# Performance work log

Measured on AMD Instinct MI355X. Metric: run time of the kernel, lower is better.

The kernel has to match this reference:

```python
import jax, jax.numpy as jnp
import numpy as np

B, N, K = 8, 2048, 20
IN_CHAN = 3
CONV_DIMS = (64, 64, 128, 256)
FEAT_DIM = 1024
SLOPE = 0.2  # LeakyReLU negative slope (DGCNN standard)


def setup_inputs() -> dict:
    key = jax.random.key(0)
    ks = jax.random.split(key, 11)
    x = jax.random.normal(ks[0], (B, N, IN_CHAN), dtype=jnp.float32)
    in_dims = (IN_CHAN,) + CONV_DIMS[:-1]
    inp = {"x": x}
    for i, (cin, cout) in enumerate(zip(in_dims, CONV_DIMS)):
        inp[f"W{i+1}"] = jax.random.normal(ks[1 + 2 * i], (cout, 2 * cin), dtype=jnp.float32) * 0.05
        inp[f"b{i+1}"] = jnp.zeros((cout,), dtype=jnp.float32)
    inp["Wf"] = jax.random.normal(ks[9], (FEAT_DIM, sum(CONV_DIMS)), dtype=jnp.float32) * 0.05
    inp["bf"] = jnp.zeros((FEAT_DIM,), dtype=jnp.float32)
    return inp


def _knn_idx(x, k):
    # x: (B, N, C) -> indices of k nearest neighbors (self included), (B, N, K)
    xx = jnp.sum(x * x, axis=-1)                       # (B, N)
    inner = jnp.einsum('bnc,bmc->bnm', x, x)           # (B, N, N)
    d2 = xx[:, :, None] - 2.0 * inner + xx[:, None, :]  # squared distances
    _, idx = jax.lax.top_k(-d2, k)                     # k smallest distances
    return idx


def _edge_conv(x, W, b, k):
    # x: (B, N, C); W: (O, 2C); b: (O,) -> (B, N, O)
    idx = _knn_idx(x, k)                               # (B, N, K)
    nbr = jax.vmap(lambda xb, ib: xb[ib])(x, idx)      # (B, N, K, C) gather
    center = jnp.broadcast_to(x[:, :, None, :], nbr.shape)
    feat = jnp.concatenate([nbr - center, center], axis=-1)  # (B, N, K, 2C)
    h = jnp.einsum('bnkc,oc->bnko', feat, W) + b       # 1x1 conv over edges
    h = jax.nn.leaky_relu(h, SLOPE)
    return jnp.max(h, axis=2)                          # max over neighbors


def reference(x, W1, b1, W2, b2, W3, b3, W4, b4, Wf, bf):
    params = [(W1, b1), (W2, b2), (W3, b3), (W4, b4)]
    feats = []
    h = x
    for W, b in params:
        h = _edge_conv(h, W, b, K)
        feats.append(h)
    hcat = jnp.concatenate(feats, axis=-1)             # (B, N, sum(conv_dims))
    out = jnp.einsum('bnc,oc->bno', hcat, Wf) + bf     # final 1x1 conv
    out = jax.nn.leaky_relu(out, SLOPE)
    return jnp.max(out, axis=1)                        # global max pool -> (B, FEAT_DIM)
```

## Files before the change

kernel.cpp:

```cpp
#include <hip/hip_runtime.h>

constexpr int B_ = 8;
constexpr int N_ = 2048;
constexpr int K_ = 20;
constexpr float SLOPE_ = 0.2f;

typedef __attribute__((ext_vector_type(8))) short bf16x8;
typedef __attribute__((ext_vector_type(8))) _Float16 f16x8;
typedef __attribute__((ext_vector_type(4))) float f32x4;

__device__ __forceinline__ float lrelu(float v) { return v > 0.0f ? v : SLOPE_ * v; }

__device__ __forceinline__ void async16(const void* g, void* l) {
  __builtin_amdgcn_global_load_lds((const __attribute__((address_space(1))) unsigned int*)g,
                                   (__attribute__((address_space(3))) unsigned int*)l, 16, 0, 0);
}

__device__ __forceinline__ unsigned long long shflx64(unsigned long long v, int m) {
  return __shfl_xor(v, m, 64);
}

__device__ __forceinline__ unsigned short f2bf(float f) {
  unsigned u = __float_as_uint(f);
  u += 0x7fff + ((u >> 16) & 1);
  return (unsigned short)(u >> 16);
}

__device__ __forceinline__ unsigned short f2h(float f) {
  _Float16 h = (_Float16)f;
  return __builtin_bit_cast(unsigned short, h);
}
__device__ __forceinline__ float h2f(unsigned short u) {
  return (float)__builtin_bit_cast(_Float16, u);
}

__global__ void prep_wp(const float* __restrict__ W, float* __restrict__ Wp, int O, int C) {
  int i = blockIdx.x * 256 + threadIdx.x;
  if (i >= 2 * O * C) return;
  int o = i / C, c = i - o * C;
  if (o < O)
    Wp[i] = W[o * 2 * C + c];
  else
    Wp[i] = W[(o - O) * 2 * C + C + c] - W[(o - O) * 2 * C + c];
}

__global__ void cvt_bf16(const float4* __restrict__ src, ushort4* __restrict__ dst, int n4) {
  int i = blockIdx.x * 256 + threadIdx.x;
  if (i >= n4) return;
  float4 v = src[i];
  ushort4 o = {f2bf(v.x), f2bf(v.y), f2bf(v.z), f2bf(v.w)};
  dst[i] = o;
}

__global__ void norms_x(const float* __restrict__ x, float* __restrict__ xx) {
  int i = blockIdx.x * 256 + threadIdx.x;
  if (i >= B_ * N_) return;
  const float* p = x + (size_t)i * 3;
  xx[i] = p[0] * p[0] + p[1] * p[1] + p[2] * p[2];
}

__global__ void split32_x(const float* __restrict__ x, unsigned short* __restrict__ xh,
                          unsigned short* __restrict__ xm) {
  int id = blockIdx.x * 256 + threadIdx.x;
  if (id >= B_ * N_ * 32) return;
  int row = id >> 5, c = id & 31;
  float val = (c < 3) ? x[row * 3 + c] : 0.0f;
  unsigned short hb = f2h(val);
  float vh = h2f(hb);
  xh[id] = hb;
  xm[id] = f2h(val - vh);
}

template <int C>
__global__ void pack_knn(const unsigned short* __restrict__ Xh,
                         const unsigned short* __restrict__ Xm,
                         unsigned short* __restrict__ Pk) {
  constexpr int KK = C / 32;
  int id = blockIdx.x * 256 + threadIdx.x;
  const int outoff = id;
  const int l = id & 63;
  id >>= 6;
  const int split = id & 1;
  id >>= 1;
  const int kk = id % KK;
  id /= KK;
  const int tile = id & 127;
  const int b = id >> 7;
  const unsigned short* src = (split == 0) ? Xh : Xm;
  const size_t soff =
      (size_t)(b * N_ + tile * 16 + (l & 15)) * C + (size_t)kk * 32 + (size_t)(l >> 4) * 8;
  uint4 v = *(const uint4*)(src + soff);
  *(uint4*)(Pk + (size_t)outoff * 8) = v;
}

__device__ __forceinline__ void select_topk(const float* __restrict__ d2row, int lane,
                                            unsigned long long* __restrict__ cb,
                                            int* __restrict__ outp) {
  float r2[32];
#pragma unroll
  for (int i = 0; i < 32; i++) r2[i] = d2row[i * 64 + lane];

  const float INF = __int_as_float(0x7f800000);

  float lmin = r2[0];
#pragma unroll
  for (int i = 1; i < 32; i++) lmin = fminf(lmin, r2[i]);
  float sv = lmin;
#pragma unroll
  for (int k = 2; k <= 64; k <<= 1)
#pragma unroll
    for (int j = k >> 1; j > 0; j >>= 1) {
      float p = __shfl_xor(sv, j, 64);
      bool takeMax = ((lane & j) != 0) == ((lane & k) == 0);
      sv = takeMax ? fmaxf(sv, p) : fminf(sv, p);
    }
  float T = __shfl(sv, 19, 64);

  unsigned cnt = 0;
#pragma unroll
  for (int i = 0; i < 32; i++) {
    bool pred = r2[i] <= T;
    unsigned long long mk = __ballot(pred);
    if (mk) {
      int off = __popcll(mk & ((1ull << lane) - 1ull));
      unsigned pos = cnt + (unsigned)off;
      if (pred && pos < 64)
        cb[pos] = ((unsigned long long)__float_as_uint(r2[i]) << 32) | (unsigned)(i * 64 + lane);
      cnt += (unsigned)__popcll(mk);
    }
  }

  if (cnt <= 64) {
    unsigned long long v = (lane < (int)cnt) ? cb[lane] : ~0ull;
#pragma unroll
    for (int k = 2; k <= 64; k <<= 1)
#pragma unroll
      for (int j = k >> 1; j > 0; j >>= 1) {
        unsigned long long p = shflx64(v, j);
        bool takeMax = ((lane & j) != 0) == ((lane & k) == 0);
        bool lt = v < p;
        v = (takeMax == lt) ? p : v;
      }
    if (lane < K_) outp[lane] = (int)(unsigned)(v & 0xffffffffull);
  } else {
    for (int t2 = 0; t2 < K_; t2++) {
      unsigned long long loc = ~0ull;
#pragma unroll
      for (int i = 0; i < 32; i++) {
        unsigned long long u =
            ((unsigned long long)__float_as_uint(r2[i]) << 32) | (unsigned)(i * 64 + lane);
        loc = u < loc ? u : loc;
      }
#pragma unroll
      for (int off = 32; off > 0; off >>= 1) {
        unsigned long long vv = shflx64(loc, off);
        loc = vv < loc ? vv : loc;
      }
      const int mwin = (int)(unsigned)(loc & 0xffffffffull);
      if (lane == 0) outp[t2] = mwin;
#pragma unroll
      for (int i = 0; i < 32; i++)
        if (i * 64 + lane == mwin) r2[i] = INF;
    }
  }
}

template <int C>
__global__ __launch_bounds__(512, 2) void knn_mfma(const unsigned short* __restrict__ Pk,
                                                   const unsigned short* __restrict__ Xh,
                                                   const unsigned short* __restrict__ Xm,
                                                   const float* __restrict__ xx,
                                                   int* __restrict__ idxo) {
  constexpr int KK = C / 32;
  constexpr int NIT = KK * 16;
  const int b = blockIdx.x & 7;
  const int q0 = (blockIdx.x >> 3) * 32;
  const int tid = threadIdx.x;
  const int w = tid >> 6, lane = tid & 63;
  const int bN = b * N_;
  const int lr = lane & 15;
  const int lk = (lane >> 4) * 8;

  __shared__ float d2s[16][2052];
  __shared__ unsigned long long cbuf[8][64];

  const size_t qoff0 = (size_t)(bN + q0 + lr) * C + lk;
  const size_t qoff1 = (size_t)(bN + q0 + 16 + lr) * C + lk;

  f32x4 acc0[16], acc1[16];
#pragma unroll
  for (int t = 0; t < 16; t++) {
    acc0[t] = (f32x4){0.0f, 0.0f, 0.0f, 0.0f};
    acc1[t] = (f32x4){0.0f, 0.0f, 0.0f, 0.0f};
  }

  const size_t pbase = (size_t)b * (128 * KK * 2 * 512) + (size_t)lane * 8;
  f16x8 bh[2], bm[2];
#pragma unroll
  for (int i = 0; i < 2; i++) {
    const size_t a = pbase + (size_t)(((w * 16 + i) * KK + 0) * 2) * 512;
    bh[i] = *(const f16x8*)(Pk + a);
    bm[i] = *(const f16x8*)(Pk + a + 512);
  }
  f16x8 ah0, am0, ah1, am1;
#pragma unroll
  for (int it = 0; it < NIT; it++) {
    const int kk = it >> 4, t = it & 15, s = it & 1;
    if (t == 0) {
      ah0 = *(const f16x8*)(Xh + qoff0 + (size_t)kk * 32);
      am0 = *(const f16x8*)(Xm + qoff0 + (size_t)kk * 32);
      ah1 = *(const f16x8*)(Xh + qoff1 + (size_t)kk * 32);
      am1 = *(const f16x8*)(Xm + qoff1 + (size_t)kk * 32);
    }
    f16x8 vh = bh[s], vm = bm[s];
    if (it + 2 < NIT) {
      const int it2 = it + 2;
      const int kk2 = it2 >> 4, t2 = it2 & 15;
      const size_t a = pbase + (size_t)(((w * 16 + t2) * KK + kk2) * 2) * 512;
      bh[s] = *(const f16x8*)(Pk + a);
      bm[s] = *(const f16x8*)(Pk + a + 512);
    }
    acc0[t] = __builtin_amdgcn_mfma_f32_16x16x32_f16(ah0, vh, acc0[t], 0, 0, 0);
    acc0[t] = __builtin_amdgcn_mfma_f32_16x16x32_f16(ah0, vm, acc0[t], 0, 0, 0);
    acc0[t] = __builtin_amdgcn_mfma_f32_16x16x32_f16(am0, vh, acc0[t], 0, 0, 0);
    acc0[t] = __builtin_amdgcn_mfma_f32_16x16x32_f16(am0, vm, acc0[t], 0, 0, 0);
    acc1[t] = __builtin_amdgcn_mfma_f32_16x16x32_f16(ah1, vh, acc1[t], 0, 0, 0);
    acc1[t] = __builtin_amdgcn_mfma_f32_16x16x32_f16(ah1, vm, acc1[t], 0, 0, 0);
    acc1[t] = __builtin_amdgcn_mfma_f32_16x16x32_f16(am1, vh, acc1[t], 0, 0, 0);
    acc1[t] = __builtin_amdgcn_mfma_f32_16x16x32_f16(am1, vm, acc1[t], 0, 0, 0);
  }

  float qn0[4], qn1[4];
#pragma unroll
  for (int r = 0; r < 4; r++) {
    qn0[r] = xx[bN + q0 + (lane >> 4) * 4 + r];
    qn1[r] = xx[bN + q0 + 16 + (lane >> 4) * 4 + r];
  }

#pragma unroll
  for (int t = 0; t < 16; t++) {
    const int tt = w * 16 + t;
    float cn = xx[bN + tt * 16 + lr];
#pragma unroll
    for (int r = 0; r < 4; r++)
      d2s[(lane >> 4) * 4 + r][tt * 16 + lr] = fmaxf(fmaf(-2.0f, acc0[t][r], cn + qn0[r]), 0.0f);
  }
  __syncthreads();
  select_topk(&d2s[2 * w + 0][0], lane, cbuf[w], idxo + (size_t)(bN + q0 + 2 * w + 0) * K_);
  select_topk(&d2s[2 * w + 1][0], lane, cbuf[w], idxo + (size_t)(bN + q0 + 2 * w + 1) * K_);
  __syncthreads();

#pragma unroll
  for (int t = 0; t < 16; t++) {
    const int tt = w * 16 + t;
    float cn = xx[bN + tt * 16 + lr];
#pragma unroll
    for (int r = 0; r < 4; r++)
      d2s[(lane >> 4) * 4 + r][tt * 16 + lr] = fmaxf(fmaf(-2.0f, acc1[t][r], cn + qn1[r]), 0.0f);
  }
  __syncthreads();
  select_topk(&d2s[2 * w + 0][0], lane, cbuf[w], idxo + (size_t)(bN + q0 + 16 + 2 * w + 0) * K_);
  select_topk(&d2s[2 * w + 1][0], lane, cbuf[w], idxo + (size_t)(bN + q0 + 16 + 2 * w + 1) * K_);
}

template <int C, int O2>
__global__ void proj_kernel(const float* __restrict__ hin, int stride,
                            const float* __restrict__ Wp, float* __restrict__ P) {
  const int nt = (blockIdx.x & 7) * N_ + (blockIdx.x >> 3) * 16;
  const int o = blockIdx.y * blockDim.x + threadIdx.x;
  __shared__ float hs[16][C];
  for (int i = threadIdx.x; i < 16 * C; i += blockDim.x) {
    int r = i / C, c = i - r * C;
    hs[r][c] = hin[(size_t)(nt + r) * stride + c];
  }
  __syncthreads();
  float acc[16];
#pragma unroll
  for (int t = 0; t < 16; t++) acc[t] = 0.0f;
  const float* wr = Wp + (size_t)o * C;
  if constexpr (C % 4 == 0) {
    for (int cg = 0; cg < C; cg += 4) {
      float4 w = *(const float4*)(wr + cg);
#pragma unroll
      for (int t = 0; t < 16; t++) {
        float4 h = *(const float4*)(&hs[t][cg]);
        acc[t] += w.x * h.x + w.y * h.y + w.z * h.z + w.w * h.w;
      }
    }
  } else {
    for (int c = 0; c < C; c++) {
      float w = wr[c];
#pragma unroll
      for (int t = 0; t < 16; t++) acc[t] += w * hs[t][c];
    }
  }
#pragma unroll
  for (int t = 0; t < 16; t++) P[(size_t)(nt + t) * O2 + o] = acc[t];
}

__global__ __launch_bounds__(256) void gemm_proj(const unsigned short* __restrict__ A, int astride,
                                                 const unsigned short* __restrict__ Bw,
                                                 float* __restrict__ P) {
  const int m0 = ((blockIdx.x & 7) * 16 + (blockIdx.x >> 3)) * 128;
  const int n0 = blockIdx.y * 128;
  const int tid = threadIdx.x;
  const int w = tid >> 6, lane = tid & 63;
  const int wm = w & 1, wn = w >> 1;

  __shared__ unsigned short lA[128 * 32];
  __shared__ unsigned short lB[128 * 32];

  const int r0 = (w * 2 + 0) * 16 + (lane >> 2);
  const int r1 = (w * 2 + 1) * 16 + (lane >> 2);
  const int ks = (lane & 3) * 8;
  const unsigned short* a0 = A + (size_t)(m0 + r0) * astride + ks;
  const unsigned short* a1 = A + (size_t)(m0 + r1) * astride + ks;
  const unsigned short* b0 = Bw + (size_t)(n0 + r0) * 128 + ks;
  const unsigned short* b1 = Bw + (size_t)(n0 + r1) * 128 + ks;
  unsigned short* lA0 = lA + (w * 2 + 0) * 512;
  unsigned short* lA1 = lA + (w * 2 + 1) * 512;
  unsigned short* lB0 = lB + (w * 2 + 0) * 512;
  unsigned short* lB1 = lB + (w * 2 + 1) * 512;

  f32x4 acc[4][4] = {};
  const int ka = (lane >> 4) * 8;

  for (int k0 = 0; k0 < 128; k0 += 32) {
    __syncthreads();
    async16(a0 + k0, lA0);
    async16(a1 + k0, lA1);
    async16(b0 + k0, lB0);
    async16(b1 + k0, lB1);
    __syncthreads();
    bf16x8 af[4], bfr[4];
#pragma unroll
    for (int mt = 0; mt < 4; mt++)
      af[mt] = *(const bf16x8*)&lA[(wm * 64 + mt * 16 + (lane & 15)) * 32 + ka];
#pragma unroll
    for (int nt = 0; nt < 4; nt++)
      bfr[nt] = *(const bf16x8*)&lB[(wn * 64 + nt * 16 + (lane & 15)) * 32 + ka];
#pragma unroll
    for (int mt = 0; mt < 4; mt++)
#pragma unroll
      for (int nt = 0; nt < 4; nt++)
        acc[mt][nt] = __builtin_amdgcn_mfma_f32_16x16x32_bf16(af[mt], bfr[nt], acc[mt][nt], 0, 0, 0);
  }

  const int col = n0 + wn * 64 + (lane & 15);
  const int rowb = m0 + wm * 64 + (lane >> 4) * 4;
#pragma unroll
  for (int mt = 0; mt < 4; mt++)
#pragma unroll
    for (int nt = 0; nt < 4; nt++)
#pragma unroll
      for (int r = 0; r < 4; r++)
        P[(size_t)(rowb + mt * 16 + r) * 512 + col + nt * 16] = acc[mt][nt][r];
}

template <int O>
__global__ __launch_bounds__(256) void combine_kernel(
    const float* __restrict__ P, const int* __restrict__ idxo, const float* __restrict__ bias,
    float* __restrict__ hout, float* __restrict__ xxo, unsigned short* __restrict__ xh,
    unsigned short* __restrict__ xm, unsigned short* __restrict__ a4) {
  constexpr int ROWS = 256 / O;
  const int bb = blockIdx.x & 7;
  const int rt = blockIdx.x >> 3;
  const int r = threadIdx.x / O;
  const int o = threadIdx.x & (O - 1);
  const int row = bb * N_ + rt * ROWS + r;
  __shared__ int idxs[ROWS][K_];
  __shared__ float ps[ROWS][O / 64 > 0 ? O / 64 : 1];
  if (o < K_) idxs[r][o] = idxo[(size_t)row * K_ + o];
  __syncthreads();
  const int base_row = bb * N_;
  float g = -3.4e38f;
#pragma unroll
  for (int k = 0; k < K_; k++) {
    float v = P[(size_t)(base_row + idxs[r][k]) * (2 * O) + o];
    g = fmaxf(g, v);
  }
  float ba = P[(size_t)row * (2 * O) + O + o];
  float val = lrelu(g + ba + bias[o]);
  hout[(size_t)row * 512 + o] = val;
  if (xh) {
    unsigned short hb = f2h(val);
    float vh = h2f(hb);
    size_t pp = (size_t)row * O + o;
    xh[pp] = hb;
    xm[pp] = f2h(val - vh);
  }
  if (a4) a4[(size_t)row * 1024 + o] = f2bf(val);
  if (xxo) {
    float sq = val * val;
#pragma unroll
    for (int off = 32; off > 0; off >>= 1) sq += __shfl_xor(sq, off, 64);
    if constexpr (O == 64) {
      if (o == 0) xxo[row] = sq;
    } else {
      if ((threadIdx.x & 63) == 0) ps[r][o >> 6] = sq;
      __syncthreads();
      if (o == 0) {
        float t = ps[r][0];
#pragma unroll
        for (int u = 1; u < O / 64; u++) t += ps[r][u];
        xxo[row] = t;
      }
    }
  }
}

__global__ __launch_bounds__(256) void gemm_final(const unsigned short* __restrict__ A,
                                                  const unsigned short* __restrict__ Bw,
                                                  float* __restrict__ part) {
  const int mt5 = (blockIdx.x & 7) * 16 + (blockIdx.x >> 3);
  const int m0 = mt5 * 128;
  const int n0 = blockIdx.y * 128;
  const int tid = threadIdx.x;
  const int w = tid >> 6, lane = tid & 63;
  const int wm = w & 1, wn = w >> 1;

  __shared__ unsigned short lA[128 * 32];
  __shared__ unsigned short lB[128 * 32];
  __shared__ float ldsred[2][128];

  const int r0 = (w * 2 + 0) * 16 + (lane >> 2);
  const int r1 = (w * 2 + 1) * 16 + (lane >> 2);
  const int ks = (lane & 3) * 8;
  const unsigned short* a0 = A + (size_t)(m0 + r0) * 512 + ks;
  const unsigned short* a1 = A + (size_t)(m0 + r1) * 512 + ks;
  const unsigned short* b0 = Bw + (size_t)(n0 + r0) * 512 + ks;
  const unsigned short* b1 = Bw + (size_t)(n0 + r1) * 512 + ks;
  unsigned short* lA0 = lA + (w * 2 + 0) * 512;
  unsigned short* lA1 = lA + (w * 2 + 1) * 512;
  unsigned short* lB0 = lB + (w * 2 + 0) * 512;
  unsigned short* lB1 = lB + (w * 2 + 1) * 512;

  f32x4 acc[4][4] = {};
  const int ka = (lane >> 4) * 8;

  for (int k0 = 0; k0 < 512; k0 += 32) {
    __syncthreads();
    async16(a0 + k0, lA0);
    async16(a1 + k0, lA1);
    async16(b0 + k0, lB0);
    async16(b1 + k0, lB1);
    __syncthreads();
    bf16x8 af[4], bfr[4];
#pragma unroll
    for (int mt = 0; mt < 4; mt++)
      af[mt] = *(const bf16x8*)&lA[(wm * 64 + mt * 16 + (lane & 15)) * 32 + ka];
#pragma unroll
    for (int nt = 0; nt < 4; nt++)
      bfr[nt] = *(const bf16x8*)&lB[(wn * 64 + nt * 16 + (lane & 15)) * 32 + ka];
#pragma unroll
    for (int mt = 0; mt < 4; mt++)
#pragma unroll
      for (int nt = 0; nt < 4; nt++)
        acc[mt][nt] = __builtin_amdgcn_mfma_f32_16x16x32_bf16(af[mt], bfr[nt], acc[mt][nt], 0, 0, 0);
  }

#pragma unroll
  for (int nt = 0; nt < 4; nt++) {
    float v = -3.4e38f;
#pragma unroll
    for (int mt = 0; mt < 4; mt++)
#pragma unroll
      for (int r = 0; r < 4; r++) v = fmaxf(v, acc[mt][nt][r]);
    v = fmaxf(v, __shfl_xor(v, 16, 64));
    v = fmaxf(v, __shfl_xor(v, 32, 64));
    if (lane < 16) ldsred[wm][wn * 64 + nt * 16 + lane] = v;
  }
  __syncthreads();
  if (tid < 128) {
    float v = fmaxf(ldsred[0][tid], ldsred[1][tid]);
    const int b = blockIdx.x & 7, s5 = blockIdx.x >> 3;
    part[(size_t)(b * 16 + s5) * 1024 + n0 + tid] = v;
  }
}

__global__ void final_reduce(const float* __restrict__ part, const float* __restrict__ bf,
                             float* __restrict__ out) {
  int i = blockIdx.x * 256 + threadIdx.x;
  if (i >= B_ * 1024) return;
  int b = i >> 10, o = i & 1023;
  float m = -3.4e38f;
  for (int s = 0; s < 16; s++) m = fmaxf(m, part[(size_t)(b * 16 + s) * 1024 + o]);
  out[i] = lrelu(m + bf[o]);
}

extern "C" void kernel_launch(void* const* d_in, const int* in_sizes, int n_in, void* d_out,
                              int out_size, void* d_ws, size_t ws_size, hipStream_t stream) {
  (void)in_sizes; (void)n_in; (void)out_size; (void)ws_size;
  const float* x = (const float*)d_in[0];
  const float* W1 = (const float*)d_in[1];
  const float* b1 = (const float*)d_in[2];
  const float* W2 = (const float*)d_in[3];
  const float* b2 = (const float*)d_in[4];
  const float* W3 = (const float*)d_in[5];
  const float* b3 = (const float*)d_in[6];
  const float* W4 = (const float*)d_in[7];
  const float* b4 = (const float*)d_in[8];
  const float* Wf = (const float*)d_in[9];
  const float* bf = (const float*)d_in[10];

  float* ws = (float*)d_ws;
  float* hcat = ws;
  float* P = hcat + (size_t)B_ * N_ * 512;
  int* idx = (int*)(P + (size_t)B_ * N_ * 512);
  float* Wp = (float*)(idx + (size_t)B_ * N_ * K_);
  float* part = Wp + 512 * 128;
  float* xxb = part + 8 * 16 * 1024;
  float* out = (float*)d_out;
  unsigned short* hcat_bf = (unsigned short*)P;
  unsigned short* Wf_bf = hcat_bf + (size_t)B_ * N_ * 512;
  unsigned short* A4_bf = (unsigned short*)hcat + 512;
  unsigned short* Wp_bf = (unsigned short*)part;

  unsigned short* Xh23 = (unsigned short*)(P + (size_t)2097152);
  unsigned short* Xm23 = Xh23 + (size_t)B_ * N_ * 64;
  unsigned short* Xh4 = (unsigned short*)(P + (size_t)4194304);
  unsigned short* Xm4 = Xh4 + (size_t)B_ * N_ * 128;
  unsigned short* Xh1 = Xh23;
  unsigned short* Xm1 = Xh1 + (size_t)B_ * N_ * 32;
  unsigned short* Pk = (unsigned short*)P;

  dim3 knng32q(N_ / 32 * B_);
  const int pk_blocks32 = B_ * 128 * 1 * 2 * 64 / 256;
  const int pk_blocks64 = B_ * 128 * 2 * 2 * 64 / 256;
  const int pk_blocks128 = B_ * 128 * 4 * 2 * 64 / 256;

  prep_wp<<<(2 * 64 * 3 + 255) / 256, 256, 0, stream>>>(W1, Wp, 64, 3);
  norms_x<<<(B_ * N_ + 255) / 256, 256, 0, stream>>>(x, xxb);
  split32_x<<<(B_ * N_ * 32 + 255) / 256, 256, 0, stream>>>(x, Xh1, Xm1);
  pack_knn<32><<<pk_blocks32, 256, 0, stream>>>(Xh1, Xm1, Pk);
  knn_mfma<32><<<knng32q, 512, 0, stream>>>(Pk, Xh1, Xm1, xxb, idx);
  proj_kernel<3, 128><<<dim3(B_ * N_ / 16, 1), 128, 0, stream>>>(x, 3, Wp, P);
  combine_kernel<64><<<B_ * N_ / 4, 256, 0, stream>>>(P, idx, b1, hcat + 0, xxb, Xh23, Xm23,
                                                      nullptr);

  prep_wp<<<(2 * 64 * 64 + 255) / 256, 256, 0, stream>>>(W2, Wp, 64, 64);
  pack_knn<64><<<pk_blocks64, 256, 0, stream>>>(Xh23, Xm23, Pk);
  knn_mfma<64><<<knng32q, 512, 0, stream>>>(Pk, Xh23, Xm23, xxb, idx);
  proj_kernel<64, 128><<<dim3(B_ * N_ / 16, 1), 128, 0, stream>>>(hcat + 0, 512, Wp, P);
  combine_kernel<64><<<B_ * N_ / 4, 256, 0, stream>>>(P, idx, b2, hcat + 64, xxb, Xh23, Xm23,
                                                      nullptr);

  prep_wp<<<(2 * 128 * 64 + 255) / 256, 256, 0, stream>>>(W3, Wp, 128, 64);
  pack_knn<64><<<pk_blocks64, 256, 0, stream>>>(Xh23, Xm23, Pk);
  knn_mfma<64><<<knng32q, 512, 0, stream>>>(Pk, Xh23, Xm23, xxb, idx);
  proj_kernel<64, 256><<<dim3(B_ * N_ / 16, 1), 256, 0, stream>>>(hcat + 64, 512, Wp, P);
  combine_kernel<128><<<B_ * N_ / 2, 256, 0, stream>>>(P, idx, b3, hcat + 128, xxb, Xh4, Xm4,
                                                       A4_bf);

  prep_wp<<<(2 * 256 * 128 + 255) / 256, 256, 0, stream>>>(W4, Wp, 256, 128);
  pack_knn<128><<<pk_blocks128, 256, 0, stream>>>(Xh4, Xm4, Pk);
  knn_mfma<128><<<knng32q, 512, 0, stream>>>(Pk, Xh4, Xm4, xxb, idx);
  cvt_bf16<<<(512 * 128 / 4 + 255) / 256, 256, 0, stream>>>(
      (const float4*)Wp, (ushort4*)Wp_bf, 512 * 128 / 4);
  gemm_proj<<<dim3(B_ * N_ / 128, 4), 256, 0, stream>>>(A4_bf, 1024, Wp_bf, P);
  combine_kernel<256><<<B_ * N_, 256, 0, stream>>>(P, idx, b4, hcat + 256, nullptr, nullptr,
                                                   nullptr, nullptr);

  cvt_bf16<<<(B_ * N_ * 512 / 4 + 255) / 256, 256, 0, stream>>>(
      (const float4*)hcat, (ushort4*)hcat_bf, B_ * N_ * 512 / 4);
  cvt_bf16<<<(1024 * 512 / 4 + 255) / 256, 256, 0, stream>>>(
      (const float4*)Wf, (ushort4*)Wf_bf, 1024 * 512 / 4);
  gemm_final<<<dim3(128, 8), 256, 0, stream>>>(hcat_bf, Wf_bf, part);
  final_reduce<<<(B_ * 1024 + 255) / 256, 256, 0, stream>>>(part, bf, out);
}
```

Before: 457.8 us.

## Add 16-query kNN kernel for layer 1 and fuse small prep kernels

Layer 1 kNN now uses a new kernel that handles 16 queries per 1024-thread block, so twice as many blocks cover the shallow C=32 case. Each wave computes 8 candidate tiles with a 3-deep register prefetch of packed candidates. The squared-norm computation moves into split32_x through a 32-lane shuffle reduction, and the bf16 weight conversion for layer 4 moves into prep_wp, which removes two kernel launches. The new kernel uses a large LDS buffer with 1024 threads, which can limit occupancy to one block per CU.

```diff
diff --git a/kernel.cpp b/kernel.cpp
--- a/kernel.cpp
+++ b/kernel.cpp
@@ -34,14 +34,18 @@
   return (float)__builtin_bit_cast(_Float16, u);
 }
 
-__global__ void prep_wp(const float* __restrict__ W, float* __restrict__ Wp, int O, int C) {
+__global__ void prep_wp(const float* __restrict__ W, float* __restrict__ Wp,
+                        unsigned short* __restrict__ Wp_bf, int O, int C) {
   int i = blockIdx.x * 256 + threadIdx.x;
   if (i >= 2 * O * C) return;
   int o = i / C, c = i - o * C;
+  float v;
   if (o < O)
-    Wp[i] = W[o * 2 * C + c];
+    v = W[o * 2 * C + c];
   else
-    Wp[i] = W[(o - O) * 2 * C + C + c] - W[(o - O) * 2 * C + c];
+    v = W[(o - O) * 2 * C + C + c] - W[(o - O) * 2 * C + c];
+  Wp[i] = v;
+  if (Wp_bf) Wp_bf[i] = f2bf(v);
 }
 
 __global__ void cvt_bf16(const float4* __restrict__ src, ushort4* __restrict__ dst, int n4) {
@@ -52,15 +56,8 @@
   dst[i] = o;
 }
 
-__global__ void norms_x(const float* __restrict__ x, float* __restrict__ xx) {
-  int i = blockIdx.x * 256 + threadIdx.x;
-  if (i >= B_ * N_) return;
-  const float* p = x + (size_t)i * 3;
-  xx[i] = p[0] * p[0] + p[1] * p[1] + p[2] * p[2];
-}
-
 __global__ void split32_x(const float* __restrict__ x, unsigned short* __restrict__ xh,
-                          unsigned short* __restrict__ xm) {
+                          unsigned short* __restrict__ xm, float* __restrict__ xx) {
   int id = blockIdx.x * 256 + threadIdx.x;
   if (id >= B_ * N_ * 32) return;
   int row = id >> 5, c = id & 31;
@@ -69,6 +66,10 @@
   float vh = h2f(hb);
   xh[id] = hb;
   xm[id] = f2h(val - vh);
+  float sq = val * val;
+#pragma unroll
+  for (int off = 16; off > 0; off >>= 1) sq += __shfl_xor(sq, off, 32);
+  if (c == 0) xx[row] = sq;
 }
 
 template <int C>
@@ -166,11 +167,87 @@
 }
 
 template <int C>
-__global__ __launch_bounds__(512, 2) void knn_mfma(const unsigned short* __restrict__ Pk,
-                                                   const unsigned short* __restrict__ Xh,
-                                                   const unsigned short* __restrict__ Xm,
-                                                   const float* __restrict__ xx,
-                                                   int* __restrict__ idxo) {
+__global__ __launch_bounds__(1024, 4) void knn_mfma_q16(const unsigned short* __restrict__ Pk,
+                                                        const unsigned short* __restrict__ Xh,
+                                                        const unsigned short* __restrict__ Xm,
+                                                        const float* __restrict__ xx,
+                                                        int* __restrict__ idxo) {
+  constexpr int KK = C / 32;
+  constexpr int DP = 3;
+  constexpr int NIT = KK * 8;
+  const int b = blockIdx.x & 7;
+  const int q0 = (blockIdx.x >> 3) * 16;
+  const int tid = threadIdx.x;
+  const int w = tid >> 6, lane = tid & 63;
+  const int bN = b * N_;
+  const int lr = lane & 15;
+  const int lk = (lane >> 4) * 8;
+
+  __shared__ float d2s[16][2052];
+  __shared__ unsigned long long cbuf[16][64];
+
+  const size_t qoff = (size_t)(bN + q0 + lr) * C + lk;
+  f16x8 a2h[2], a2m[2];
+  a2h[0] = *(const f16x8*)(Xh + qoff);
+  a2m[0] = *(const f16x8*)(Xm + qoff);
+
+  f32x4 acc[8];
+#pragma unroll
+  for (int t = 0; t < 8; t++) acc[t] = (f32x4){0.0f, 0.0f, 0.0f, 0.0f};
+
+  const size_t pbase = (size_t)b * (128 * KK * 2 * 512) + (size_t)lane * 8;
+  f16x8 bh[DP], bm[DP];
+#pragma unroll
+  for (int i = 0; i < DP; i++) {
+    const size_t a = pbase + (size_t)(((w * 8 + i) * KK + 0) * 2) * 512;
+    bh[i] = *(const f16x8*)(Pk + a);
+    bm[i] = *(const f16x8*)(Pk + a + 512);
+  }
+#pragma unroll
+  for (int it = 0; it < NIT; it++) {
+    const int kk = it >> 3, t = it & 7, s = it % DP;
+    if (t == 0 && kk + 1 < KK) {
+      const size_t qa = qoff + (size_t)(kk + 1) * 32;
+      a2h[(kk + 1) & 1] = *(const f16x8*)(Xh + qa);
+      a2m[(kk + 1) & 1] = *(const f16x8*)(Xm + qa);
+    }
+    f16x8 vh = bh[s], vm = bm[s];
+    if (it + DP < NIT) {
+      const int it2 = it + DP;
+      const int kk2 = it2 >> 3, t2 = it2 & 7;
+      const size_t a = pbase + (size_t)(((w * 8 + t2) * KK + kk2) * 2) * 512;
+      bh[s] = *(const f16x8*)(Pk + a);
+      bm[s] = *(const f16x8*)(Pk + a + 512);
+    }
+    const f16x8 ah = a2h[kk & 1], am = a2m[kk & 1];
+    acc[t] = __builtin_amdgcn_mfma_f32_16x16x32_f16(ah, vh, acc[t], 0, 0, 0);
+    acc[t] = __builtin_amdgcn_mfma_f32_16x16x32_f16(ah, vm, acc[t], 0, 0, 0);
+    acc[t] = __builtin_amdgcn_mfma_f32_16x16x32_f16(am, vh, acc[t], 0, 0, 0);
+    acc[t] = __builtin_amdgcn_mfma_f32_16x16x32_f16(am, vm, acc[t], 0, 0, 0);
+  }
+
+  float qn[4];
+#pragma unroll
+  for (int r = 0; r < 4; r++) qn[r] = xx[bN + q0 + (lane >> 4) * 4 + r];
+#pragma unroll
+  for (int t = 0; t < 8; t++) {
+    float cn = xx[bN + (w * 8 + t) * 16 + lr];
+#pragma unroll
+    for (int r = 0; r < 4; r++) {
+      float v = fmaxf(fmaf(-2.0f, acc[t][r], cn + qn[r]), 0.0f);
+      d2s[(lane >> 4) * 4 + r][(w * 8 + t) * 16 + lr] = v;
+    }
+  }
+  __syncthreads();
+  select_topk(&d2s[w][0], lane, cbuf[w], idxo + (size_t)(bN + q0 + w) * K_);
+}
+
+template <int C>
+__global__ __launch_bounds__(512, 2) void knn_mfma_q32(const unsigned short* __restrict__ Pk,
+                                                       const unsigned short* __restrict__ Xh,
+                                                       const unsigned short* __restrict__ Xm,
+                                                       const float* __restrict__ xx,
+                                                       int* __restrict__ idxo) {
   constexpr int KK = C / 32;
   constexpr int NIT = KK * 16;
   const int b = blockIdx.x & 7;
@@ -524,39 +601,37 @@
   unsigned short* Xm1 = Xh1 + (size_t)B_ * N_ * 32;
   unsigned short* Pk = (unsigned short*)P;
 
+  dim3 knng16(N_ / 16 * B_);
   dim3 knng32q(N_ / 32 * B_);
   const int pk_blocks32 = B_ * 128 * 1 * 2 * 64 / 256;
   const int pk_blocks64 = B_ * 128 * 2 * 2 * 64 / 256;
   const int pk_blocks128 = B_ * 128 * 4 * 2 * 64 / 256;
 
-  prep_wp<<<(2 * 64 * 3 + 255) / 256, 256, 0, stream>>>(W1, Wp, 64, 3);
-  norms_x<<<(B_ * N_ + 255) / 256, 256, 0, stream>>>(x, xxb);
-  split32_x<<<(B_ * N_ * 32 + 255) / 256, 256, 0, stream>>>(x, Xh1, Xm1);
+  prep_wp<<<(2 * 64 * 3 + 255) / 256, 256, 0, stream>>>(W1, Wp, nullptr, 64, 3);
+  split32_x<<<(B_ * N_ * 32 + 255) / 256, 256, 0, stream>>>(x, Xh1, Xm1, xxb);
   pack_knn<32><<<pk_blocks32, 256, 0, stream>>>(Xh1, Xm1, Pk);
-  knn_mfma<32><<<knng32q, 512, 0, stream>>>(Pk, Xh1, Xm1, xxb, idx);
+  knn_mfma_q16<32><<<knng16, 1024, 0, stream>>>(Pk, Xh1, Xm1, xxb, idx);
   proj_kernel<3, 128><<<dim3(B_ * N_ / 16, 1), 128, 0, stream>>>(x, 3, Wp, P);
   combine_kernel<64><<<B_ * N_ / 4, 256, 0, stream>>>(P, idx, b1, hcat + 0, xxb, Xh23, Xm23,
                                                       nullptr);
 
-  prep_wp<<<(2 * 64 * 64 + 255) / 256, 256, 0, stream>>>(W2, Wp, 64, 64);
+  prep_wp<<<(2 * 64 * 64 + 255) / 256, 256, 0, stream>>>(W2, Wp, nullptr, 64, 64);
   pack_knn<64><<<pk_blocks64, 256, 0, stream>>>(Xh23, Xm23, Pk);
-  knn_mfma<64><<<knng32q, 512, 0, stream>>>(Pk, Xh23, Xm23, xxb, idx);
+  knn_mfma_q32<64><<<knng32q, 512, 0, stream>>>(Pk, Xh23, Xm23, xxb, idx);
   proj_kernel<64, 128><<<dim3(B_ * N_ / 16, 1), 128, 0, stream>>>(hcat + 0, 512, Wp, P);
   combine_kernel<64><<<B_ * N_ / 4, 256, 0, stream>>>(P, idx, b2, hcat + 64, xxb, Xh23, Xm23,
                                                       nullptr);
 
-  prep_wp<<<(2 * 128 * 64 + 255) / 256, 256, 0, stream>>>(W3, Wp, 128, 64);
+  prep_wp<<<(2 * 128 * 64 + 255) / 256, 256, 0, stream>>>(W3, Wp, nullptr, 128, 64);
   pack_knn<64><<<pk_blocks64, 256, 0, stream>>>(Xh23, Xm23, Pk);
-  knn_mfma<64><<<knng32q, 512, 0, stream>>>(Pk, Xh23, Xm23, xxb, idx);
+  knn_mfma_q32<64><<<knng32q, 512, 0, stream>>>(Pk, Xh23, Xm23, xxb, idx);
   proj_kernel<64, 256><<<dim3(B_ * N_ / 16, 1), 256, 0, stream>>>(hcat + 64, 512, Wp, P);
   combine_kernel<128><<<B_ * N_ / 2, 256, 0, stream>>>(P, idx, b3, hcat + 128, xxb, Xh4, Xm4,
                                                        A4_bf);
 
-  prep_wp<<<(2 * 256 * 128 + 255) / 256, 256, 0, stream>>>(W4, Wp, 256, 128);
+  prep_wp<<<(2 * 256 * 128 + 255) / 256, 256, 0, stream>>>(W4, Wp, Wp_bf, 256, 128);
   pack_knn<128><<<pk_blocks128, 256, 0, stream>>>(Xh4, Xm4, Pk);
-  knn_mfma<128><<<knng32q, 512, 0, stream>>>(Pk, Xh4, Xm4, xxb, idx);
-  cvt_bf16<<<(512 * 128 / 4 + 255) / 256, 256, 0, stream>>>(
-      (const float4*)Wp, (ushort4*)Wp_bf, 512 * 128 / 4);
+  knn_mfma_q32<128><<<knng32q, 512, 0, stream>>>(Pk, Xh4, Xm4, xxb, idx);
   gemm_proj<<<dim3(B_ * N_ / 128, 4), 256, 0, stream>>>(A4_bf, 1024, Wp_bf, P);
   combine_kernel<256><<<B_ * N_, 256, 0, stream>>>(P, idx, b4, hcat + 256, nullptr, nullptr,
                                                    nullptr, nullptr);
```

New measurement: 446.1 us. 2.6% less time.
